# Kernel tuning notes

Measured on AMD Instinct MI355X. Metric: run time of the kernel, lower is better.

Reference implementation:

```python
import jax, jax.numpy as jnp
import numpy as np
from jax import lax

B, T = 32, 1500
E, D, A, C, K, O = 512, 512, 512, 10, 100, 512
SCALING = 2.0


def setup_inputs() -> dict:
    key = jax.random.key(0)
    ks = jax.random.split(key, 12)
    inp = {
        "enc_pad": jax.random.normal(ks[0], (B, T, E), dtype=jnp.float32),
        "enc_len": jnp.full((B,), T, dtype=jnp.int32),
        "dec_z": jax.random.normal(ks[1], (B, D), dtype=jnp.float32),
        "att_prev": jax.random.uniform(ks[2], (B, T), dtype=jnp.float32) / T,
        # parameters (Linear weights stored as [in, out] for x @ W)
        "W_enc": jax.random.normal(ks[3], (E, A), dtype=jnp.float32) * (1.0 / np.sqrt(E)),
        "b_enc": jnp.zeros((A,), dtype=jnp.float32),
        "W_dec": jax.random.normal(ks[4], (D, A), dtype=jnp.float32) * (1.0 / np.sqrt(D)),
        "W_att": jax.random.normal(ks[5], (C, A), dtype=jnp.float32) * (1.0 / np.sqrt(C)),
        "conv_w": jax.random.normal(ks[6], (C, 1, 2 * K + 1), dtype=jnp.float32) * 0.05,  # OIH
        "gvec_w": jax.random.normal(ks[7], (A,), dtype=jnp.float32) * (1.0 / np.sqrt(A)),
        "W_o": jax.random.normal(ks[8], (E, O), dtype=jnp.float32) * (1.0 / np.sqrt(E)),
        "b_o": jnp.zeros((O,), dtype=jnp.float32),
    }
    return inp


def reference(enc_pad, enc_len, dec_z, att_prev, W_enc, b_enc, W_dec, W_att,
              conv_w, gvec_w, W_o, b_o):
    # pre_compute_enc_h = mlp_enc(enc_h): [B, T, A]
    pre_enc = jnp.einsum("bte,ea->bta", enc_pad, W_enc) + b_enc
    # location conv over previous attention weights: [B,1,T] -> [B,C,T]
    att_conv = lax.conv_general_dilated(
        att_prev[:, None, :], conv_w,
        window_strides=(1,), padding=[(K, K)],
        dimension_numbers=("NCH", "OIH", "NCH"))
    # [B, T, C] -> mlp_att -> [B, T, A]
    att_conv = jnp.einsum("bct,ca->bta", att_conv, W_att)
    # dec projection tiled: [B, 1, A]
    dec_tiled = (dec_z @ W_dec)[:, None, :]
    att_state = jnp.tanh(pre_enc + dec_tiled + att_conv)  # [B, T, A]
    e = jnp.einsum("bta,a->bt", att_state, gvec_w)          # [B, T]
    w = jax.nn.softmax(SCALING * e, axis=1)                  # [B, T]
    c = jnp.einsum("bt,bte->be", w, enc_pad)                 # [B, E]
    c = c @ W_o + b_o                                        # [B, O]
    return (c, w)
```

## Files before the change

kernel.cpp:

```cpp
#include <hip/hip_runtime.h>
#include <hip/hip_bf16.h>

#define B_  32
#define T_  1500
#define C_  10
#define KH  100
#define KW  201
#define M_  48000
#define KP  544
#define SCALING_ 2.0f
#define BT_BYTES 17408
#define C2L 2.8853900817779268f

typedef __bf16 bf16;
typedef __attribute__((ext_vector_type(8))) __bf16 bf16x8;
typedef __attribute__((ext_vector_type(4))) float f32x4;

__device__ __forceinline__ void load_lds16(const void* g, void* l) {
    __builtin_amdgcn_global_load_lds(
        (const __attribute__((address_space(1))) unsigned int*)g,
        (__attribute__((address_space(3))) unsigned int*)l,
        16, 0, 0);
}

__global__ void prep_bias(const float* __restrict__ dec_z, const float* __restrict__ W_dec,
                          const float* __restrict__ b_enc, float* __restrict__ biasC) {
    int idx = blockIdx.x * 256 + threadIdx.x;
    int b = idx >> 9, a = idx & 511;
    float acc = b_enc[a];
#pragma unroll 8
    for (int d = 0; d < 512; ++d)
        acc += dec_z[b * 512 + d] * W_dec[d * 512 + a];
    biasC[idx] = acc * C2L;
}

__global__ void gsum_k(const float* __restrict__ g, float* __restrict__ gsum) {
    __shared__ float red[256];
    int h = blockIdx.x, tid = threadIdx.x;
    red[tid] = g[h * 256 + tid];
    __syncthreads();
    for (int st = 128; st > 0; st >>= 1) {
        if (tid < st) red[tid] += red[tid + st];
        __syncthreads();
    }
    if (tid == 0) gsum[h] = red[0];
}

__global__ void prep_wt(const float* __restrict__ W_enc, const float* __restrict__ W_att,
                        bf16* __restrict__ wt2) {
    int k = blockIdx.x;
    int s = k >> 3, j = k & 7;
    for (int a = threadIdx.x; a < 512; a += 256) {
        float v;
        if (k < 512)       v = W_enc[k * 512 + a];
        else if (k < 522)  v = W_att[(k - 512) * 512 + a];
        else               v = 0.0f;
        int nt = a >> 4, c = a & 15;
        wt2[((nt * 68 + s) * 16 + c) * 8 + j] = (bf16)v;
    }
}

__global__ void prep_conv(const float* __restrict__ att_prev, const float* __restrict__ conv_w,
                          bf16* __restrict__ convpad) {
    int tc = blockIdx.x;
    int b  = blockIdx.y;
    int tid = threadIdx.x;
    __shared__ float s_att[456];
    __shared__ float s_w[C_ * KW];
    int t0 = tc * 256;
    for (int i = tid; i < 456; i += 256) {
        int ti = t0 - KH + i;
        s_att[i] = (ti >= 0 && ti < T_) ? att_prev[b * T_ + ti] : 0.0f;
    }
    for (int i = tid; i < C_ * KW; i += 256) s_w[i] = conv_w[i];
    __syncthreads();
    int t = t0 + tid;
    if (t < T_) {
        float acc[C_];
#pragma unroll
        for (int c = 0; c < C_; ++c) acc[c] = 0.0f;
        for (int j = 0; j < KW; ++j) {
            float a = s_att[tid + j];
#pragma unroll
            for (int c = 0; c < C_; ++c) acc[c] += a * s_w[c * KW + j];
        }
        bf16* dst = convpad + (size_t)(b * T_ + t) * 32;
#pragma unroll
        for (int c = 0; c < C_; ++c) dst[c] = (bf16)acc[c];
#pragma unroll
        for (int c = C_; c < 32; ++c) dst[c] = (bf16)0.0f;
    }
}

__global__ __launch_bounds__(256, 2) void main_gemm(
        const float* __restrict__ enc, const bf16* __restrict__ convpad,
        const bf16* __restrict__ wt2, const float* __restrict__ biasC,
        const float* __restrict__ gvec, const float* __restrict__ gsum,
        float* __restrict__ e_out) {
    __shared__ __align__(16) char b_lds[2 * BT_BYTES];
    __shared__ float biasL[2][256];
    __shared__ float gvL[256];
    const int tid  = threadIdx.x;
    const int lane = tid & 63;
    const int wid  = tid >> 6;
    const int g    = lane >> 4;
    const int c15  = lane & 15;
    const int bid  = blockIdx.x;
    const int nh   = bid & 1;
    const int rc   = bid >> 1;
    const int rowbase = rc * 128 + wid * 32;
    const int nbase   = nh * 256;

    {
        int b0 = (rc * 128) / T_, b1 = (rc * 128 + 127) / T_;
        biasL[0][tid] = biasC[b0 * 512 + nbase + tid];
        biasL[1][tid] = biasC[b1 * 512 + nbase + tid];
        gvL[tid]      = gvec[nbase + tid];
    }

    bf16x8 afrag[2][16];
#pragma unroll
    for (int m = 0; m < 2; ++m) {
        const float* ap = enc + (size_t)(rowbase + m * 16 + c15) * 512 + g * 8;
#pragma unroll
        for (int kt = 0; kt < 16; ++kt) {
            float4 f0 = *(const float4*)(ap + kt * 32);
            float4 f1 = *(const float4*)(ap + kt * 32 + 4);
            bf16x8 v;
            v[0] = (bf16)f0.x; v[1] = (bf16)f0.y; v[2] = (bf16)f0.z; v[3] = (bf16)f0.w;
            v[4] = (bf16)f1.x; v[5] = (bf16)f1.y; v[6] = (bf16)f1.z; v[7] = (bf16)f1.w;
            afrag[m][kt] = v;
        }
    }
    bf16x8 acv[2];
#pragma unroll
    for (int m = 0; m < 2; ++m)
        acv[m] = *(const bf16x8*)(convpad + (size_t)(rowbase + m * 16 + c15) * 32 + g * 8);

    int bsel[2][4];
    {
        int b0lim = ((rc * 128) / T_ + 1) * T_;
#pragma unroll
        for (int m = 0; m < 2; ++m)
#pragma unroll
            for (int r = 0; r < 4; ++r)
                bsel[m][r] = (rowbase + m * 16 + g * 4 + r >= b0lim) ? 256 : 0;
    }

    {
        const char* src = (const char*)wt2 + (size_t)(nh * 16) * BT_BYTES;
#pragma unroll
        for (int p = 0; p < 4; ++p) {
            int q = wid + p * 4;
            load_lds16(src + q * 1024 + lane * 16, b_lds + q * 1024);
        }
        if (wid == 0) load_lds16(src + 16 * 1024 + lane * 16, b_lds + 16 * 1024);
    }

    const int lane_off = g * 256 + c15 * 16;
    const float* blf = &biasL[0][0];
    float su[2][4] = {{0.f,0.f,0.f,0.f},{0.f,0.f,0.f,0.f}};

    for (int nt = 0; nt < 16; ++nt) {
        __syncthreads();
        if (nt < 15) {
            const char* src = (const char*)wt2 + (size_t)(nh * 16 + nt + 1) * BT_BYTES;
            char* dst = b_lds + ((nt + 1) & 1) * BT_BYTES;
#pragma unroll
            for (int p = 0; p < 4; ++p) {
                int q = wid + p * 4;
                load_lds16(src + q * 1024 + lane * 16, dst + q * 1024);
            }
            if (wid == 0) load_lds16(src + 16 * 1024 + lane * 16, dst + 16 * 1024);
        }
        const char* bb = b_lds + (nt & 1) * BT_BYTES + lane_off;
        f32x4 acc0 = {0.f, 0.f, 0.f, 0.f};
        f32x4 acc1 = {0.f, 0.f, 0.f, 0.f};
#pragma unroll
        for (int kt = 0; kt < 16; ++kt) {
            bf16x8 bv = *(const bf16x8*)(bb + kt * 1024);
            acc0 = __builtin_amdgcn_mfma_f32_16x16x32_bf16(afrag[0][kt], bv, acc0, 0, 0, 0);
            acc1 = __builtin_amdgcn_mfma_f32_16x16x32_bf16(afrag[1][kt], bv, acc1, 0, 0, 0);
        }
        {
            bf16x8 bv = *(const bf16x8*)(bb + 16 * 1024);
            acc0 = __builtin_amdgcn_mfma_f32_16x16x32_bf16(acv[0], bv, acc0, 0, 0, 0);
            acc1 = __builtin_amdgcn_mfma_f32_16x16x32_bf16(acv[1], bv, acc1, 0, 0, 0);
        }
        int nloc = nt * 16 + c15;
        float gv = gvL[nloc];
#pragma unroll
        for (int m = 0; m < 2; ++m) {
            f32x4 a = m ? acc1 : acc0;
#pragma unroll
            for (int r = 0; r < 4; ++r) {
                float t  = fmaf(a[r], C2L, blf[bsel[m][r] + nloc]);
                float ex = exp2f(t);
                float u  = __builtin_amdgcn_rcpf(ex + 1.0f);
                su[m][r] = fmaf(gv, u, su[m][r]);
            }
        }
    }
#pragma unroll
    for (int msk = 1; msk < 16; msk <<= 1)
#pragma unroll
        for (int m = 0; m < 2; ++m)
#pragma unroll
            for (int r = 0; r < 4; ++r)
                su[m][r] += __shfl_xor(su[m][r], msk, 64);
    if (c15 == 0) {
        float gs = gsum[nh];
#pragma unroll
        for (int m = 0; m < 2; ++m)
#pragma unroll
            for (int r = 0; r < 4; ++r)
                atomicAdd(e_out + rowbase + m * 16 + g * 4 + r,
                          gs - 2.0f * su[m][r]);
    }
}

__global__ void softmax_k(const float* __restrict__ e_in, float* __restrict__ w_out) {
    int b = blockIdx.x, tid = threadIdx.x;
    __shared__ float red[256];
    float v[6];
    float mx = -1e30f;
#pragma unroll
    for (int i = 0; i < 6; ++i) {
        int t = i * 256 + tid;
        v[i] = (t < T_) ? SCALING_ * e_in[b * T_ + t] : -1e30f;
        mx = fmaxf(mx, v[i]);
    }
    red[tid] = mx; __syncthreads();
    for (int st = 128; st > 0; st >>= 1) {
        if (tid < st) red[tid] = fmaxf(red[tid], red[tid + st]);
        __syncthreads();
    }
    mx = red[0]; __syncthreads();
    float sum = 0.f;
#pragma unroll
    for (int i = 0; i < 6; ++i) { v[i] = __expf(v[i] - mx); sum += v[i]; }
    red[tid] = sum; __syncthreads();
    for (int st = 128; st > 0; st >>= 1) {
        if (tid < st) red[tid] += red[tid + st];
        __syncthreads();
    }
    float inv = 1.0f / red[0];
#pragma unroll
    for (int i = 0; i < 6; ++i) {
        int t = i * 256 + tid;
        if (t < T_) w_out[b * T_ + t] = v[i] * inv;
    }
}

__global__ void ctx_partial(const float* __restrict__ enc, const float* __restrict__ w,
                            float* __restrict__ partial) {
    int e  = blockIdx.x * 256 + threadIdx.x;
    int ty = blockIdx.y;
    int b  = blockIdx.z;
    int t0 = ty * 94;
    int t1 = min(t0 + 94, T_);
    float acc = 0.f;
#pragma unroll 8
    for (int t = t0; t < t1; ++t)
        acc += w[b * T_ + t] * enc[((size_t)b * T_ + t) * 512 + e];
    partial[(ty * 32 + b) * 512 + e] = acc;
}

__global__ void out_proj(const float* __restrict__ partial, const float* __restrict__ Wo,
                         const float* __restrict__ bo, float* __restrict__ out) {
    int b = blockIdx.x, half = blockIdx.y, tid = threadIdx.x;
    __shared__ float ctx[512];
    for (int e = tid; e < 512; e += 256) {
        float s = 0.f;
#pragma unroll
        for (int p = 0; p < 16; ++p) s += partial[(p * 32 + b) * 512 + e];
        ctx[e] = s;
    }
    __syncthreads();
    int o = half * 256 + tid;
    float a0 = bo[o];
#pragma unroll 8
    for (int e = 0; e < 512; ++e)
        a0 += ctx[e] * Wo[e * 512 + o];
    out[b * 512 + o] = a0;
}

extern "C" void kernel_launch(void* const* d_in, const int* in_sizes, int n_in,
                              void* d_out, int out_size, void* d_ws, size_t ws_size,
                              hipStream_t stream) {
    const float* enc      = (const float*)d_in[0];
    const float* dec_z    = (const float*)d_in[2];
    const float* att_prev = (const float*)d_in[3];
    const float* W_enc    = (const float*)d_in[4];
    const float* b_enc    = (const float*)d_in[5];
    const float* W_dec    = (const float*)d_in[6];
    const float* W_att    = (const float*)d_in[7];
    const float* conv_w   = (const float*)d_in[8];
    const float* gvec     = (const float*)d_in[9];
    const float* W_o      = (const float*)d_in[10];
    const float* b_o      = (const float*)d_in[11];

    char* ws = (char*)d_ws;
    float* biasC   = (float*)(ws);
    float* e_buf   = (float*)(ws + 65536);
    float* gsum    = (float*)(ws + 257536);
    float* partial = (float*)(ws);
    bf16*  convpad = (bf16*)(ws + 1048576);
    bf16*  wt2     = (bf16*)(ws + 4120576);

    float* c_out = (float*)d_out;
    float* w_out = c_out + B_ * 512;

    prep_bias<<<64, 256, 0, stream>>>(dec_z, W_dec, b_enc, biasC);
    gsum_k<<<2, 256, 0, stream>>>(gvec, gsum);
    prep_wt<<<KP, 256, 0, stream>>>(W_enc, W_att, wt2);
    prep_conv<<<dim3(6, B_), 256, 0, stream>>>(att_prev, conv_w, convpad);
    hipMemsetAsync(e_buf, 0, M_ * sizeof(float), stream);
    main_gemm<<<750, 256, 0, stream>>>(enc, convpad, wt2, biasC, gvec, gsum, e_buf);
    softmax_k<<<B_, 256, 0, stream>>>(e_buf, w_out);
    ctx_partial<<<dim3(2, 16, B_), 256, 0, stream>>>(enc, w_out, partial);
    out_proj<<<dim3(B_, 2), 256, 0, stream>>>(partial, W_o, b_o, c_out);
}
```

Measured before the change: 316.6 us.

## Fuse prep kernels, drop atomics and memset, vectorize context reduction

The three preprocessing kernels (bias projection, weight repacking, location conv) are merged into one block-dispatched launch, and the gvec-sum kernel is removed by folding the constant into softmax, where it cancels under the max subtraction. main_gemm now writes per-half partial scores to separate buffers instead of using atomicAdd, which removes the memset, and softmax adds the two halves. ctx_partial and out_proj are rewritten to use float4 loads with an in-block reduction, and main_gemm's launch bounds request 3 blocks per SM. These cut launch count and atomic traffic, but the occupancy hint may force register spills.

```diff
diff --git a/kernel.cpp b/kernel.cpp
--- a/kernel.cpp
+++ b/kernel.cpp
@@ -23,80 +23,76 @@
         16, 0, 0);
 }
 
-__global__ void prep_bias(const float* __restrict__ dec_z, const float* __restrict__ W_dec,
-                          const float* __restrict__ b_enc, float* __restrict__ biasC) {
-    int idx = blockIdx.x * 256 + threadIdx.x;
-    int b = idx >> 9, a = idx & 511;
-    float acc = b_enc[a];
-#pragma unroll 8
-    for (int d = 0; d < 512; ++d)
-        acc += dec_z[b * 512 + d] * W_dec[d * 512 + a];
-    biasC[idx] = acc * C2L;
-}
-
-__global__ void gsum_k(const float* __restrict__ g, float* __restrict__ gsum) {
-    __shared__ float red[256];
-    int h = blockIdx.x, tid = threadIdx.x;
-    red[tid] = g[h * 256 + tid];
-    __syncthreads();
-    for (int st = 128; st > 0; st >>= 1) {
-        if (tid < st) red[tid] += red[tid + st];
+__global__ void fused_prep(const float* __restrict__ dec_z, const float* __restrict__ W_dec,
+                           const float* __restrict__ b_enc, float* __restrict__ biasC,
+                           const float* __restrict__ W_enc, const float* __restrict__ W_att,
+                           bf16* __restrict__ wt2,
+                           const float* __restrict__ att_prev, const float* __restrict__ conv_w,
+                           bf16* __restrict__ convpad) {
+    __shared__ float smem[2466];
+    const int bid = blockIdx.x;
+    const int tid = threadIdx.x;
+
+    if (bid < 64) {
+        int idx = bid * 256 + tid;
+        int b = idx >> 9, a = idx & 511;
+        float acc = b_enc[a];
+#pragma unroll 16
+        for (int d = 0; d < 512; ++d)
+            acc += dec_z[b * 512 + d] * W_dec[d * 512 + a];
+        biasC[idx] = acc * C2L;
+    } else if (bid < 200) {
+        int idx = (bid - 64) * 256 + tid;
+        int nt = idx / 1088;
+        int rem = idx - nt * 1088;
+        int s = rem >> 4, c = rem & 15;
+        int a = nt * 16 + c;
+        bf16x8 vv;
+#pragma unroll
+        for (int j = 0; j < 8; ++j) {
+            int k = s * 8 + j;
+            float v;
+            if (k < 512)       v = W_enc[k * 512 + a];
+            else if (k < 522)  v = W_att[(k - 512) * 512 + a];
+            else               v = 0.0f;
+            vv[j] = (bf16)v;
+        }
+        *(bf16x8*)(wt2 + (size_t)idx * 8) = vv;
+    } else {
+        int cb = bid - 200;
+        int tc = cb % 6, b = cb / 6;
+        float* s_att = smem;
+        float* s_w   = smem + 456;
+        int t0 = tc * 256;
+        for (int i = tid; i < 456; i += 256) {
+            int ti = t0 - KH + i;
+            s_att[i] = (ti >= 0 && ti < T_) ? att_prev[b * T_ + ti] : 0.0f;
+        }
+        for (int i = tid; i < C_ * KW; i += 256) s_w[i] = conv_w[i];
         __syncthreads();
-    }
-    if (tid == 0) gsum[h] = red[0];
-}
-
-__global__ void prep_wt(const float* __restrict__ W_enc, const float* __restrict__ W_att,
-                        bf16* __restrict__ wt2) {
-    int k = blockIdx.x;
-    int s = k >> 3, j = k & 7;
-    for (int a = threadIdx.x; a < 512; a += 256) {
-        float v;
-        if (k < 512)       v = W_enc[k * 512 + a];
-        else if (k < 522)  v = W_att[(k - 512) * 512 + a];
-        else               v = 0.0f;
-        int nt = a >> 4, c = a & 15;
-        wt2[((nt * 68 + s) * 16 + c) * 8 + j] = (bf16)v;
-    }
-}
-
-__global__ void prep_conv(const float* __restrict__ att_prev, const float* __restrict__ conv_w,
-                          bf16* __restrict__ convpad) {
-    int tc = blockIdx.x;
-    int b  = blockIdx.y;
-    int tid = threadIdx.x;
-    __shared__ float s_att[456];
-    __shared__ float s_w[C_ * KW];
-    int t0 = tc * 256;
-    for (int i = tid; i < 456; i += 256) {
-        int ti = t0 - KH + i;
-        s_att[i] = (ti >= 0 && ti < T_) ? att_prev[b * T_ + ti] : 0.0f;
-    }
-    for (int i = tid; i < C_ * KW; i += 256) s_w[i] = conv_w[i];
-    __syncthreads();
-    int t = t0 + tid;
-    if (t < T_) {
-        float acc[C_];
-#pragma unroll
-        for (int c = 0; c < C_; ++c) acc[c] = 0.0f;
-        for (int j = 0; j < KW; ++j) {
-            float a = s_att[tid + j];
-#pragma unroll
-            for (int c = 0; c < C_; ++c) acc[c] += a * s_w[c * KW + j];
-        }
-        bf16* dst = convpad + (size_t)(b * T_ + t) * 32;
-#pragma unroll
-        for (int c = 0; c < C_; ++c) dst[c] = (bf16)acc[c];
-#pragma unroll
-        for (int c = C_; c < 32; ++c) dst[c] = (bf16)0.0f;
-    }
-}
-
-__global__ __launch_bounds__(256, 2) void main_gemm(
+        int t = t0 + tid;
+        if (t < T_) {
+            float acc[C_];
+#pragma unroll
+            for (int c = 0; c < C_; ++c) acc[c] = 0.0f;
+            for (int j = 0; j < KW; ++j) {
+                float a = s_att[tid + j];
+#pragma unroll
+                for (int c = 0; c < C_; ++c) acc[c] += a * s_w[c * KW + j];
+            }
+            bf16* dst = convpad + (size_t)(b * T_ + t) * 32;
+#pragma unroll
+            for (int c = 0; c < C_; ++c) dst[c] = (bf16)acc[c];
+#pragma unroll
+            for (int c = C_; c < 32; ++c) dst[c] = (bf16)0.0f;
+        }
+    }
+}
+
+__global__ __launch_bounds__(256, 3) void main_gemm(
         const float* __restrict__ enc, const bf16* __restrict__ convpad,
         const bf16* __restrict__ wt2, const float* __restrict__ biasC,
-        const float* __restrict__ gvec, const float* __restrict__ gsum,
-        float* __restrict__ e_out) {
+        const float* __restrict__ gvec, float* __restrict__ e_part) {
     __shared__ __align__(16) char b_lds[2 * BT_BYTES];
     __shared__ float biasL[2][256];
     __shared__ float gvL[256];
@@ -209,17 +205,15 @@
             for (int r = 0; r < 4; ++r)
                 su[m][r] += __shfl_xor(su[m][r], msk, 64);
     if (c15 == 0) {
-        float gs = gsum[nh];
 #pragma unroll
         for (int m = 0; m < 2; ++m)
 #pragma unroll
             for (int r = 0; r < 4; ++r)
-                atomicAdd(e_out + rowbase + m * 16 + g * 4 + r,
-                          gs - 2.0f * su[m][r]);
-    }
-}
-
-__global__ void softmax_k(const float* __restrict__ e_in, float* __restrict__ w_out) {
+                e_part[nh * M_ + rowbase + m * 16 + g * 4 + r] = su[m][r];
+    }
+}
+
+__global__ void softmax_k(const float* __restrict__ e_part, float* __restrict__ w_out) {
     int b = blockIdx.x, tid = threadIdx.x;
     __shared__ float red[256];
     float v[6];
@@ -227,7 +221,10 @@
 #pragma unroll
     for (int i = 0; i < 6; ++i) {
         int t = i * 256 + tid;
-        v[i] = (t < T_) ? SCALING_ * e_in[b * T_ + t] : -1e30f;
+        if (t < T_) {
+            float s2 = e_part[b * T_ + t] + e_part[M_ + b * T_ + t];
+            v[i] = -2.0f * SCALING_ * s2;
+        } else v[i] = -1e30f;
         mx = fmaxf(mx, v[i]);
     }
     red[tid] = mx; __syncthreads();
@@ -254,32 +251,50 @@
 
 __global__ void ctx_partial(const float* __restrict__ enc, const float* __restrict__ w,
                             float* __restrict__ partial) {
-    int e  = blockIdx.x * 256 + threadIdx.x;
-    int ty = blockIdx.y;
-    int b  = blockIdx.z;
+    int ty = blockIdx.x;
+    int b  = blockIdx.y;
+    int tid = threadIdx.x;
+    int half = tid >> 7;
+    int cq   = tid & 127;
     int t0 = ty * 94;
     int t1 = min(t0 + 94, T_);
-    float acc = 0.f;
-#pragma unroll 8
-    for (int t = t0; t < t1; ++t)
-        acc += w[b * T_ + t] * enc[((size_t)b * T_ + t) * 512 + e];
-    partial[(ty * 32 + b) * 512 + e] = acc;
+    f32x4 acc = {0.f, 0.f, 0.f, 0.f};
+    for (int t = t0 + half; t < t1; t += 2) {
+        float wt = w[b * T_ + t];
+        f32x4 ev = *(const f32x4*)(enc + ((size_t)(b * T_ + t) << 9) + cq * 4);
+        acc.x = fmaf(wt, ev.x, acc.x);
+        acc.y = fmaf(wt, ev.y, acc.y);
+        acc.z = fmaf(wt, ev.z, acc.z);
+        acc.w = fmaf(wt, ev.w, acc.w);
+    }
+    __shared__ f32x4 red[256];
+    red[tid] = acc;
+    __syncthreads();
+    if (tid < 128) {
+        f32x4 s = red[tid];
+        f32x4 o = red[tid + 128];
+        s.x += o.x; s.y += o.y; s.z += o.z; s.w += o.w;
+        *(f32x4*)(partial + ((size_t)(ty * 32 + b) << 9) + tid * 4) = s;
+    }
 }
 
 __global__ void out_proj(const float* __restrict__ partial, const float* __restrict__ Wo,
                          const float* __restrict__ bo, float* __restrict__ out) {
     int b = blockIdx.x, half = blockIdx.y, tid = threadIdx.x;
     __shared__ float ctx[512];
-    for (int e = tid; e < 512; e += 256) {
-        float s = 0.f;
-#pragma unroll
-        for (int p = 0; p < 16; ++p) s += partial[(p * 32 + b) * 512 + e];
-        ctx[e] = s;
+    if (tid < 128) {
+        f32x4 s = {0.f, 0.f, 0.f, 0.f};
+#pragma unroll
+        for (int p = 0; p < 16; ++p) {
+            f32x4 v = *(const f32x4*)(partial + ((size_t)(p * 32 + b) << 9) + tid * 4);
+            s.x += v.x; s.y += v.y; s.z += v.z; s.w += v.w;
+        }
+        *(f32x4*)(ctx + tid * 4) = s;
     }
     __syncthreads();
     int o = half * 256 + tid;
     float a0 = bo[o];
-#pragma unroll 8
+#pragma unroll 16
     for (int e = 0; e < 512; ++e)
         a0 += ctx[e] * Wo[e * 512 + o];
     out[b * 512 + o] = a0;
@@ -302,8 +317,7 @@
 
     char* ws = (char*)d_ws;
     float* biasC   = (float*)(ws);
-    float* e_buf   = (float*)(ws + 65536);
-    float* gsum    = (float*)(ws + 257536);
+    float* e_part  = (float*)(ws + 65536);
     float* partial = (float*)(ws);
     bf16*  convpad = (bf16*)(ws + 1048576);
     bf16*  wt2     = (bf16*)(ws + 4120576);
@@ -311,13 +325,11 @@
     float* c_out = (float*)d_out;
     float* w_out = c_out + B_ * 512;
 
-    prep_bias<<<64, 256, 0, stream>>>(dec_z, W_dec, b_enc, biasC);
-    gsum_k<<<2, 256, 0, stream>>>(gvec, gsum);
-    prep_wt<<<KP, 256, 0, stream>>>(W_enc, W_att, wt2);
-    prep_conv<<<dim3(6, B_), 256, 0, stream>>>(att_prev, conv_w, convpad);
-    hipMemsetAsync(e_buf, 0, M_ * sizeof(float), stream);
-    main_gemm<<<750, 256, 0, stream>>>(enc, convpad, wt2, biasC, gvec, gsum, e_buf);
-    softmax_k<<<B_, 256, 0, stream>>>(e_buf, w_out);
-    ctx_partial<<<dim3(2, 16, B_), 256, 0, stream>>>(enc, w_out, partial);
+    fused_prep<<<392, 256, 0, stream>>>(dec_z, W_dec, b_enc, biasC,
+                                        W_enc, W_att, wt2,
+                                        att_prev, conv_w, convpad);
+    main_gemm<<<750, 256, 0, stream>>>(enc, convpad, wt2, biasC, gvec, e_part);
+    softmax_k<<<B_, 256, 0, stream>>>(e_part, w_out);
+    ctx_partial<<<dim3(16, B_), 256, 0, stream>>>(enc, w_out, partial);
     out_proj<<<dim3(B_, 2), 256, 0, stream>>>(partial, W_o, b_o, c_out);
 }
```

Measured after the change: 311.2 us. Within noise of the previous version (-1.7%).
